# Kernel optimization log

Measured on AMD Instinct MI355X. Metric: run time of the kernel, lower is better.

## Reference

```python
import jax, jax.numpy as jnp
import numpy as np

HIDDEN = 192
NDIM = 3
N_NODES = 262144
BATCH = 8
N_SUPER = 2048
DEG = 16
N_EDGES = BATCH * N_SUPER * DEG  # 262144
MAX_WAVELENGTH = 10000.0


def sincos_embed(coords):
    # ContinuousSincosEmbed: dim=192, ndim=3 -> 64 dims per coord (32 sin + 32 cos), no padding
    d_per = HIDDEN // NDIM  # 64
    omega = 1.0 / MAX_WAVELENGTH ** (jnp.arange(0, d_per, 2, dtype=jnp.float32) / d_per)  # [32]
    out = coords[:, :, None] * omega[None, None, :]            # [N, ndim, 32]
    emb = jnp.concatenate([jnp.sin(out), jnp.cos(out)], -1)    # [N, ndim, 64]
    return emb.reshape(coords.shape[0], HIDDEN)                # [N, 192]


def _xavier(key, fan_in, fan_out):
    bound = np.sqrt(6.0 / (fan_in + fan_out)).astype(np.float32)
    return jax.random.uniform(key, (fan_in, fan_out), jnp.float32, -bound, bound)


def setup_inputs() -> dict:
    key = jax.random.key(0)
    k = jax.random.split(key, 8)
    mesh_pos = jax.random.normal(k[0], (N_NODES, NDIM), jnp.float32)
    # edges grouped by sorted dst (segment_csr precondition); every supernode appears DEG times
    dst = jnp.repeat(jnp.arange(BATCH * N_SUPER, dtype=jnp.int32), DEG)          # [E]
    src = jax.random.randint(k[1], (N_EDGES,), 0, N_NODES, dtype=jnp.int32)      # [E]
    mesh_edges = jnp.stack([dst, src], axis=1)                                   # [E, 2]
    batch_idx = jnp.repeat(jnp.arange(BATCH, dtype=jnp.int32), N_NODES // BATCH)
    return {
        "mesh_pos": mesh_pos,
        "mesh_edges": mesh_edges,
        "batch_idx": batch_idx,
        "W1": _xavier(k[2], 2 * HIDDEN, 2 * HIDDEN), "b1": jnp.zeros((2 * HIDDEN,), jnp.float32),
        "W2": _xavier(k[3], 2 * HIDDEN, HIDDEN),     "b2": jnp.zeros((HIDDEN,), jnp.float32),
        "W3": _xavier(k[4], HIDDEN, HIDDEN),         "b3": jnp.zeros((HIDDEN,), jnp.float32),
    }


def reference(mesh_pos, mesh_edges, batch_idx, W1, b1, W2, b2, W3, b3):
    x = sincos_embed(mesh_pos)                       # [N, H]
    dst_idx = mesh_edges[:, 0]
    src_idx = mesh_edges[:, 1]
    h = jnp.concatenate([x[src_idx], x[dst_idx]], axis=1)        # [E, 2H]
    h = jax.nn.gelu(h @ W1 + b1, approximate=False)
    h = jax.nn.gelu(h @ W2 + b2, approximate=False)
    h = h @ W3 + b3                                              # [E, H]
    num_segments = BATCH * N_SUPER  # = number of unique dst by construction
    sums = jax.ops.segment_sum(h, dst_idx, num_segments=num_segments)
    counts = jax.ops.segment_sum(jnp.ones((h.shape[0],), h.dtype), dst_idx,
                                 num_segments=num_segments)
    mean = sums / jnp.maximum(counts, 1.0)[:, None]              # segment_csr mean
    return mean.reshape(BATCH, N_SUPER, HIDDEN)
```

## Files before the change

### kernel.cpp

```cpp
#include <hip/hip_runtime.h>

#define HID    192
#define HID2   384
#define NEDGES 262144
#define NSEG   16384
#define MB     64
#define NBLK   (NEDGES / MB)

#define ALD   200
#define H1LD  408
#define MH2   26112
#define SMEM2 26880

typedef __bf16 bf16;
typedef __bf16 bv8 __attribute__((ext_vector_type(8)));
typedef __bf16 bv4 __attribute__((ext_vector_type(4)));
typedef float f32x4 __attribute__((ext_vector_type(4)));

__device__ __forceinline__ float gelu_fast(float x) {
    float x2 = x * x;
    float u2 = 1.5957691216057308f * x * __builtin_fmaf(0.044715f, x2, 1.0f);
    float e  = __expf(u2);
    float inv = __builtin_amdgcn_rcpf(e + 1.0f);
    return __builtin_fmaf(-x, inv, x);
}

__device__ __forceinline__ bv8 embed8(float p0, float p1, float p2, int t0) {
    const int dim   = t0 >> 6;
    const int isCos = t0 & 32;
    const int f0    = t0 & 31;
    const float pv  = (dim == 0) ? p0 : ((dim == 1) ? p1 : p2);
    float om = exp2f(-0.4152410118609203f * (float)f0);
    bv8 v;
    #pragma unroll
    for (int j = 0; j < 8; ++j) {
        const float x = pv * om;
        v[j] = (bf16)(isCos ? __cosf(x) : __sinf(x));
        om *= 0.74989420933245582f;
    }
    return v;
}

__global__ __launch_bounds__(256)
void prep_kernel(const float* __restrict__ W1, const float* __restrict__ W2,
                 const float* __restrict__ W3,
                 const float* __restrict__ pos, const int* __restrict__ edges,
                 bf16* __restrict__ W1T, bf16* __restrict__ W2T, bf16* __restrict__ W3T,
                 bf16* __restrict__ dstC) {
    if (blockIdx.x < 252) {
        __shared__ float t[32][33];
        int b = blockIdx.x;
        const float* S; bf16* D; int K, N, tk, tn;
        if (b < 144)      { S = W1; D = W1T; K = 384; N = 384; tk = (b / 12) * 32; tn = (b % 12) * 32; }
        else if (b < 216) { b -= 144; S = W2; D = W2T; K = 384; N = 192; tk = (b / 6) * 32; tn = (b % 6) * 32; }
        else              { b -= 216; S = W3; D = W3T; K = 192; N = 192; tk = (b / 6) * 32; tn = (b % 6) * 32; }
        const int c = threadIdx.x & 31, r0 = threadIdx.x >> 5;
        #pragma unroll
        for (int i = 0; i < 4; ++i)
            t[r0 + i * 8][c] = S[(size_t)(tk + r0 + i * 8) * N + tn + c];
        __syncthreads();
        #pragma unroll
        for (int i = 0; i < 4; ++i)
            D[(size_t)(tn + r0 + i * 8) * K + tk + c] = (bf16)t[c][r0 + i * 8];
        return;
    }
    __shared__ __align__(16) bf16 smem[MB * ALD];
    const int tid = threadIdx.x, w = tid >> 6, lane = tid & 63;
    const int quad = lane >> 4, l15 = lane & 15;
    const int blk = blockIdx.x - 252;
    {
        const int r = tid >> 2, part = tid & 3;
        const int node = edges[2 * ((blk * MB + r) * 16)];
        const float p0 = pos[node * 3 + 0], p1 = pos[node * 3 + 1], p2 = pos[node * 3 + 2];
        bf16* ldst = smem + r * ALD + part * 48;
        #pragma unroll
        for (int g = 0; g < 6; ++g)
            *reinterpret_cast<bv8*>(ldst + g * 8) = embed8(p0, p1, p2, part * 48 + g * 8);
    }
    __syncthreads();
    const f32x4 fz = {0.f, 0.f, 0.f, 0.f};
    f32x4 acc[6][4];
    #pragma unroll
    for (int mc = 0; mc < 6; ++mc)
        #pragma unroll
        for (int ne = 0; ne < 4; ++ne) acc[mc][ne] = fz;
    const bf16* xb = smem + l15 * ALD + quad * 8;
    for (int kt = 0; kt < 6; ++kt) {
        bv8 x[4];
        #pragma unroll
        for (int ne = 0; ne < 4; ++ne)
            x[ne] = *reinterpret_cast<const bv8*>(xb + ne * 16 * ALD + kt * 32);
        #pragma unroll
        for (int mc = 0; mc < 6; ++mc) {
            bv8 a;
            const int col = w * 96 + mc * 16 + l15;
            #pragma unroll
            for (int j = 0; j < 8; ++j)
                a[j] = (bf16)W1[(size_t)(192 + kt * 32 + quad * 8 + j) * HID2 + col];
            #pragma unroll
            for (int ne = 0; ne < 4; ++ne)
                acc[mc][ne] = __builtin_amdgcn_mfma_f32_16x16x32_bf16(a, x[ne], acc[mc][ne], 0, 0, 0);
        }
    }
    #pragma unroll
    for (int mc = 0; mc < 6; ++mc)
        #pragma unroll
        for (int ne = 0; ne < 4; ++ne) {
            bv4 pk;
            #pragma unroll
            for (int r = 0; r < 4; ++r) pk[r] = (bf16)acc[mc][ne][r];
            *reinterpret_cast<bv4*>(dstC + (size_t)(blk * MB + ne * 16 + l15) * HID2
                                    + w * 96 + mc * 16 + quad * 4) = pk;
        }
}

__global__ __launch_bounds__(256, 3)
void fused_mlp_kernel(const float* __restrict__ pos, const int* __restrict__ edges,
                      const bf16* __restrict__ W1T, const float* __restrict__ b1,
                      const bf16* __restrict__ W2T, const float* __restrict__ b2,
                      const bf16* __restrict__ W3T, const float* __restrict__ b3,
                      const bf16* __restrict__ dstC, float* __restrict__ out) {
    __shared__ __align__(16) bf16 smem[SMEM2];
    const int tid = threadIdx.x, w = tid >> 6, lane = tid & 63;
    const int quad = lane >> 4, l15 = lane & 15, blk = blockIdx.x;

    {
        const int r = tid >> 2, part = tid & 3;
        const int node = edges[2 * (blk * MB + r) + 1];
        const float p0 = pos[node * 3 + 0], p1 = pos[node * 3 + 1], p2 = pos[node * 3 + 2];
        bf16* ldst = smem + r * ALD + part * 48;
        #pragma unroll
        for (int g = 0; g < 6; ++g)
            *reinterpret_cast<bv8*>(ldst + g * 8) = embed8(p0, p1, p2, part * 48 + g * 8);
    }
    __syncthreads();

    const f32x4 fz = {0.f, 0.f, 0.f, 0.f};

    f32x4 acc1[6][4];
    #pragma unroll
    for (int mc = 0; mc < 6; ++mc)
        #pragma unroll
        for (int ne = 0; ne < 4; ++ne) acc1[mc][ne] = fz;
    {
        const bf16* wb = W1T + (size_t)(w * 96 + l15) * HID2 + quad * 8;
        const bf16* xb = smem + l15 * ALD + quad * 8;
        for (int kt = 0; kt < 6; ++kt) {
            bv8 x[4];
            #pragma unroll
            for (int ne = 0; ne < 4; ++ne)
                x[ne] = *reinterpret_cast<const bv8*>(xb + ne * 16 * ALD + kt * 32);
            #pragma unroll
            for (int mc = 0; mc < 6; ++mc) {
                bv8 a = *reinterpret_cast<const bv8*>(wb + mc * 16 * HID2 + kt * 32);
                #pragma unroll
                for (int ne = 0; ne < 4; ++ne)
                    acc1[mc][ne] = __builtin_amdgcn_mfma_f32_16x16x32_bf16(a, x[ne], acc1[mc][ne], 0, 0, 0);
            }
        }
    }
    __syncthreads();

    {
        #pragma unroll
        for (int mc = 0; mc < 6; ++mc) {
            const int cb = w * 96 + mc * 16 + quad * 4;
            f32x4 bia = *reinterpret_cast<const f32x4*>(b1 + cb);
            #pragma unroll
            for (int ne = 0; ne < 4; ++ne) {
                bv4 dc = *reinterpret_cast<const bv4*>(dstC + (size_t)(blk * 4 + ne) * HID2 + cb);
                bv4 o;
                #pragma unroll
                for (int r = 0; r < 4; ++r)
                    o[r] = (bf16)gelu_fast(acc1[mc][ne][r] + (float)dc[r] + bia[r]);
                *reinterpret_cast<bv4*>(smem + (ne * 16 + l15) * H1LD + cb) = o;
            }
        }
    }
    __syncthreads();

    f32x4 acc2[4][3];
    #pragma unroll
    for (int m = 0; m < 4; ++m)
        #pragma unroll
        for (int nc = 0; nc < 3; ++nc) acc2[m][nc] = fz;
    {
        const bf16* hb = smem + l15 * H1LD + quad * 8;
        const bf16* wb = W2T + (size_t)(w * 48 + l15) * HID2 + quad * 8;
        for (int kt = 0; kt < 12; ++kt) {
            bv8 h[4];
            #pragma unroll
            for (int m = 0; m < 4; ++m)
                h[m] = *reinterpret_cast<const bv8*>(hb + m * 16 * H1LD + kt * 32);
            #pragma unroll
            for (int nc = 0; nc < 3; ++nc) {
                bv8 b = *reinterpret_cast<const bv8*>(wb + nc * 16 * HID2 + kt * 32);
                #pragma unroll
                for (int m = 0; m < 4; ++m)
                    acc2[m][nc] = __builtin_amdgcn_mfma_f32_16x16x32_bf16(h[m], b, acc2[m][nc], 0, 0, 0);
            }
        }
    }

    #pragma unroll
    for (int nc = 0; nc < 3; ++nc) {
        const int colv = w * 48 + nc * 16 + l15;
        const float bia = b2[colv];
        #pragma unroll
        for (int m = 0; m < 4; ++m) {
            float s = gelu_fast(acc2[m][nc][0] + bia) + gelu_fast(acc2[m][nc][1] + bia)
                    + gelu_fast(acc2[m][nc][2] + bia) + gelu_fast(acc2[m][nc][3] + bia);
            s += __shfl_xor(s, 16);
            s += __shfl_xor(s, 32);
            if (quad == 0)
                smem[MH2 + m * HID + colv] = (bf16)(s * 0.0625f);
        }
    }
    __syncthreads();

    {
        f32x4 acc3[3];
        #pragma unroll
        for (int nc = 0; nc < 3; ++nc) acc3[nc] = fz;
        const bf16* ab = smem + MH2 + (l15 & 3) * HID + quad * 8;
        const bf16* wb = W3T + (size_t)(w * 48 + l15) * HID + quad * 8;
        for (int kt = 0; kt < 6; ++kt) {
            bv8 a = *reinterpret_cast<const bv8*>(ab + kt * 32);
            #pragma unroll
            for (int nc = 0; nc < 3; ++nc) {
                bv8 b = *reinterpret_cast<const bv8*>(wb + nc * 16 * HID + kt * 32);
                acc3[nc] = __builtin_amdgcn_mfma_f32_16x16x32_bf16(a, b, acc3[nc], 0, 0, 0);
            }
        }
        if (quad == 0) {
            #pragma unroll
            for (int nc = 0; nc < 3; ++nc) {
                const int col   = w * 48 + nc * 16 + l15;
                const float bia = b3[col];
                #pragma unroll
                for (int r = 0; r < 4; ++r)
                    out[(size_t)(blk * 4 + r) * HID + col] = acc3[nc][r] + bia;
            }
        }
    }
}

extern "C" void kernel_launch(void* const* d_in, const int* in_sizes, int n_in,
                              void* d_out, int out_size, void* d_ws, size_t ws_size,
                              hipStream_t stream) {
    const float* mesh_pos = (const float*)d_in[0];
    const int*   edges    = (const int*)  d_in[1];
    const float* W1 = (const float*)d_in[3];
    const float* b1 = (const float*)d_in[4];
    const float* W2 = (const float*)d_in[5];
    const float* b2 = (const float*)d_in[6];
    const float* W3 = (const float*)d_in[7];
    const float* b3 = (const float*)d_in[8];
    float* out = (float*)d_out;

    bf16* W1T  = (bf16*)d_ws;
    bf16* W2T  = W1T + 147456;
    bf16* W3T  = W2T + 73728;
    bf16* dstC = W3T + 36864;

    prep_kernel<<<508, 256, 0, stream>>>(W1, W2, W3, mesh_pos, edges, W1T, W2T, W3T, dstC);
    fused_mlp_kernel<<<NBLK, 256, 0, stream>>>(mesh_pos, edges, W1T, b1, W2T, b2, W3T, b3,
                                               dstC, out);
}
```

Measured before the change: 276.8 us.

## Split dst-embedding prep into smaller blocks, pair sin/cos, hoist global loads

The prep kernel now gives each block 16 supernodes instead of 64, launching four times as many small blocks for the destination-side layer-1 projection. Sine and cosine are computed together from one shared argument in the embedding, in both kernels. In the fused MLP kernel, the dstC, b1, b2, b3 and W3 loads are issued before the barriers so their global latency overlaps with other work. Keeping all of W3 in registers raises VGPR pressure under the 3-block occupancy bound and may cause spills, and the smaller prep blocks re-read the fp32 W1 gather more often.

New measurement: 294.3 us. +6.3%, slower.

```diff
diff --git a/kernel.cpp b/kernel.cpp
--- a/kernel.cpp
+++ b/kernel.cpp
@@ -25,20 +25,21 @@
     return __builtin_fmaf(-x, inv, x);
 }
 
-__device__ __forceinline__ bv8 embed8(float p0, float p1, float p2, int t0) {
-    const int dim   = t0 >> 6;
-    const int isCos = t0 & 32;
-    const int f0    = t0 & 31;
-    const float pv  = (dim == 0) ? p0 : ((dim == 1) ? p1 : p2);
+__device__ __forceinline__ void embed_pair(bf16* row, float p0, float p1, float p2, int a0) {
+    const int dim = a0 >> 5;
+    const int f0  = a0 & 31;
+    const float pv = (dim == 0) ? p0 : ((dim == 1) ? p1 : p2);
     float om = exp2f(-0.4152410118609203f * (float)f0);
-    bv8 v;
+    bv8 sv, cv;
     #pragma unroll
     for (int j = 0; j < 8; ++j) {
         const float x = pv * om;
-        v[j] = (bf16)(isCos ? __cosf(x) : __sinf(x));
+        sv[j] = (bf16)__sinf(x);
+        cv[j] = (bf16)__cosf(x);
         om *= 0.74989420933245582f;
     }
-    return v;
+    *reinterpret_cast<bv8*>(row + dim * 64 + f0)      = sv;
+    *reinterpret_cast<bv8*>(row + dim * 64 + 32 + f0) = cv;
 }
 
 __global__ __launch_bounds__(256)
@@ -64,32 +65,27 @@
             D[(size_t)(tn + r0 + i * 8) * K + tk + c] = (bf16)t[c][r0 + i * 8];
         return;
     }
-    __shared__ __align__(16) bf16 smem[MB * ALD];
+    __shared__ __align__(16) bf16 smem[16 * ALD];
     const int tid = threadIdx.x, w = tid >> 6, lane = tid & 63;
     const int quad = lane >> 4, l15 = lane & 15;
-    const int blk = blockIdx.x - 252;
-    {
-        const int r = tid >> 2, part = tid & 3;
-        const int node = edges[2 * ((blk * MB + r) * 16)];
+    const int s0 = (blockIdx.x - 252) * 16;
+    if (tid < 64) {
+        const int r = tid >> 2, p = tid & 3;
+        const int node = edges[2 * ((s0 + r) * 16)];
         const float p0 = pos[node * 3 + 0], p1 = pos[node * 3 + 1], p2 = pos[node * 3 + 2];
-        bf16* ldst = smem + r * ALD + part * 48;
-        #pragma unroll
-        for (int g = 0; g < 6; ++g)
-            *reinterpret_cast<bv8*>(ldst + g * 8) = embed8(p0, p1, p2, part * 48 + g * 8);
+        bf16* row = smem + r * ALD;
+        #pragma unroll
+        for (int g = 0; g < 3; ++g)
+            embed_pair(row, p0, p1, p2, p * 24 + g * 8);
     }
     __syncthreads();
     const f32x4 fz = {0.f, 0.f, 0.f, 0.f};
-    f32x4 acc[6][4];
-    #pragma unroll
-    for (int mc = 0; mc < 6; ++mc)
-        #pragma unroll
-        for (int ne = 0; ne < 4; ++ne) acc[mc][ne] = fz;
+    f32x4 acc[6];
+    #pragma unroll
+    for (int mc = 0; mc < 6; ++mc) acc[mc] = fz;
     const bf16* xb = smem + l15 * ALD + quad * 8;
     for (int kt = 0; kt < 6; ++kt) {
-        bv8 x[4];
-        #pragma unroll
-        for (int ne = 0; ne < 4; ++ne)
-            x[ne] = *reinterpret_cast<const bv8*>(xb + ne * 16 * ALD + kt * 32);
+        bv8 x = *reinterpret_cast<const bv8*>(xb + kt * 32);
         #pragma unroll
         for (int mc = 0; mc < 6; ++mc) {
             bv8 a;
@@ -97,21 +93,17 @@
             #pragma unroll
             for (int j = 0; j < 8; ++j)
                 a[j] = (bf16)W1[(size_t)(192 + kt * 32 + quad * 8 + j) * HID2 + col];
-            #pragma unroll
-            for (int ne = 0; ne < 4; ++ne)
-                acc[mc][ne] = __builtin_amdgcn_mfma_f32_16x16x32_bf16(a, x[ne], acc[mc][ne], 0, 0, 0);
-        }
-    }
-    #pragma unroll
-    for (int mc = 0; mc < 6; ++mc)
-        #pragma unroll
-        for (int ne = 0; ne < 4; ++ne) {
-            bv4 pk;
-            #pragma unroll
-            for (int r = 0; r < 4; ++r) pk[r] = (bf16)acc[mc][ne][r];
-            *reinterpret_cast<bv4*>(dstC + (size_t)(blk * MB + ne * 16 + l15) * HID2
-                                    + w * 96 + mc * 16 + quad * 4) = pk;
-        }
+            acc[mc] = __builtin_amdgcn_mfma_f32_16x16x32_bf16(a, x, acc[mc], 0, 0, 0);
+        }
+    }
+    #pragma unroll
+    for (int mc = 0; mc < 6; ++mc) {
+        bv4 pk;
+        #pragma unroll
+        for (int r = 0; r < 4; ++r) pk[r] = (bf16)acc[mc][r];
+        *reinterpret_cast<bv4*>(dstC + (size_t)(s0 + l15) * HID2
+                                + w * 96 + mc * 16 + quad * 4) = pk;
+    }
 }
 
 __global__ __launch_bounds__(256, 3)
@@ -125,13 +117,13 @@
     const int quad = lane >> 4, l15 = lane & 15, blk = blockIdx.x;
 
     {
-        const int r = tid >> 2, part = tid & 3;
+        const int r = tid >> 2, p = tid & 3;
         const int node = edges[2 * (blk * MB + r) + 1];
         const float p0 = pos[node * 3 + 0], p1 = pos[node * 3 + 1], p2 = pos[node * 3 + 2];
-        bf16* ldst = smem + r * ALD + part * 48;
-        #pragma unroll
-        for (int g = 0; g < 6; ++g)
-            *reinterpret_cast<bv8*>(ldst + g * 8) = embed8(p0, p1, p2, part * 48 + g * 8);
+        bf16* row = smem + r * ALD;
+        #pragma unroll
+        for (int g = 0; g < 3; ++g)
+            embed_pair(row, p0, p1, p2, p * 24 + g * 8);
     }
     __syncthreads();
 
@@ -159,24 +151,35 @@
             }
         }
     }
-    __syncthreads();
-
-    {
-        #pragma unroll
-        for (int mc = 0; mc < 6; ++mc) {
-            const int cb = w * 96 + mc * 16 + quad * 4;
-            f32x4 bia = *reinterpret_cast<const f32x4*>(b1 + cb);
-            #pragma unroll
-            for (int ne = 0; ne < 4; ++ne) {
-                bv4 dc = *reinterpret_cast<const bv4*>(dstC + (size_t)(blk * 4 + ne) * HID2 + cb);
-                bv4 o;
-                #pragma unroll
-                for (int r = 0; r < 4; ++r)
-                    o[r] = (bf16)gelu_fast(acc1[mc][ne][r] + (float)dc[r] + bia[r]);
-                *reinterpret_cast<bv4*>(smem + (ne * 16 + l15) * H1LD + cb) = o;
-            }
-        }
-    }
+
+    bv4  dcH[6][4];
+    f32x4 b1H[6];
+    #pragma unroll
+    for (int mc = 0; mc < 6; ++mc) {
+        const int cb = w * 96 + mc * 16 + quad * 4;
+        b1H[mc] = *reinterpret_cast<const f32x4*>(b1 + cb);
+        #pragma unroll
+        for (int ne = 0; ne < 4; ++ne)
+            dcH[mc][ne] = *reinterpret_cast<const bv4*>(dstC + (size_t)(blk * 4 + ne) * HID2 + cb);
+    }
+    __syncthreads();
+
+    #pragma unroll
+    for (int mc = 0; mc < 6; ++mc) {
+        const int cb = w * 96 + mc * 16 + quad * 4;
+        #pragma unroll
+        for (int ne = 0; ne < 4; ++ne) {
+            bv4 o;
+            #pragma unroll
+            for (int r = 0; r < 4; ++r)
+                o[r] = (bf16)gelu_fast(acc1[mc][ne][r] + (float)dcH[mc][ne][r] + b1H[mc][r]);
+            *reinterpret_cast<bv4*>(smem + (ne * 16 + l15) * H1LD + cb) = o;
+        }
+    }
+
+    float b2H[3];
+    #pragma unroll
+    for (int nc = 0; nc < 3; ++nc) b2H[nc] = b2[w * 48 + nc * 16 + l15];
     __syncthreads();
 
     f32x4 acc2[4][3];
@@ -205,17 +208,29 @@
     #pragma unroll
     for (int nc = 0; nc < 3; ++nc) {
         const int colv = w * 48 + nc * 16 + l15;
-        const float bia = b2[colv];
         #pragma unroll
         for (int m = 0; m < 4; ++m) {
-            float s = gelu_fast(acc2[m][nc][0] + bia) + gelu_fast(acc2[m][nc][1] + bia)
-                    + gelu_fast(acc2[m][nc][2] + bia) + gelu_fast(acc2[m][nc][3] + bia);
+            float s = gelu_fast(acc2[m][nc][0] + b2H[nc]) + gelu_fast(acc2[m][nc][1] + b2H[nc])
+                    + gelu_fast(acc2[m][nc][2] + b2H[nc]) + gelu_fast(acc2[m][nc][3] + b2H[nc]);
             s += __shfl_xor(s, 16);
             s += __shfl_xor(s, 32);
             if (quad == 0)
                 smem[MH2 + m * HID + colv] = (bf16)(s * 0.0625f);
         }
     }
+
+    bv8 w3H[3][6];
+    {
+        const bf16* wb = W3T + (size_t)(w * 48 + l15) * HID + quad * 8;
+        #pragma unroll
+        for (int nc = 0; nc < 3; ++nc)
+            #pragma unroll
+            for (int kt = 0; kt < 6; ++kt)
+                w3H[nc][kt] = *reinterpret_cast<const bv8*>(wb + nc * 16 * HID + kt * 32);
+    }
+    float b3H[3];
+    #pragma unroll
+    for (int nc = 0; nc < 3; ++nc) b3H[nc] = b3[w * 48 + nc * 16 + l15];
     __syncthreads();
 
     {
@@ -223,23 +238,19 @@
         #pragma unroll
         for (int nc = 0; nc < 3; ++nc) acc3[nc] = fz;
         const bf16* ab = smem + MH2 + (l15 & 3) * HID + quad * 8;
-        const bf16* wb = W3T + (size_t)(w * 48 + l15) * HID + quad * 8;
         for (int kt = 0; kt < 6; ++kt) {
             bv8 a = *reinterpret_cast<const bv8*>(ab + kt * 32);
             #pragma unroll
+            for (int nc = 0; nc < 3; ++nc)
+                acc3[nc] = __builtin_amdgcn_mfma_f32_16x16x32_bf16(a, w3H[nc][kt], acc3[nc], 0, 0, 0);
+        }
+        if (quad == 0) {
+            #pragma unroll
             for (int nc = 0; nc < 3; ++nc) {
-                bv8 b = *reinterpret_cast<const bv8*>(wb + nc * 16 * HID + kt * 32);
-                acc3[nc] = __builtin_amdgcn_mfma_f32_16x16x32_bf16(a, b, acc3[nc], 0, 0, 0);
-            }
-        }
-        if (quad == 0) {
-            #pragma unroll
-            for (int nc = 0; nc < 3; ++nc) {
-                const int col   = w * 48 + nc * 16 + l15;
-                const float bia = b3[col];
+                const int col = w * 48 + nc * 16 + l15;
                 #pragma unroll
                 for (int r = 0; r < 4; ++r)
-                    out[(size_t)(blk * 4 + r) * HID + col] = acc3[nc][r] + bia;
+                    out[(size_t)(blk * 4 + r) * HID + col] = acc3[nc][r] + b3H[nc];
             }
         }
     }
@@ -263,7 +274,8 @@
     bf16* W3T  = W2T + 73728;
     bf16* dstC = W3T + 36864;
 
-    prep_kernel<<<508, 256, 0, stream>>>(W1, W2, W3, mesh_pos, edges, W1T, W2T, W3T, dstC);
+    prep_kernel<<<252 + NSEG / 16, 256, 0, stream>>>(W1, W2, W3, mesh_pos, edges,
+                                                     W1T, W2T, W3T, dstC);
     fused_mlp_kernel<<<NBLK, 256, 0, stream>>>(mesh_pos, edges, W1T, b1, W2T, b2, W3T, b3,
                                                dstC, out);
 }
```
